# Kernel optimization log

Hardware: AMD Instinct MI355X
Metric: run time of the kernel (lower is better)

## Reference

```python
import jax, jax.numpy as jnp
import numpy as np

BN_EPS = 1e-5
CLUSTER_SIZE = 32  # K (real clusters kept after softmax)


def setup_inputs() -> dict:
    key = jax.random.key(0)
    ks = jax.random.split(key, 7)
    B, N, D, Ktot, K = 4096, 128, 512, 48, 32
    x = jax.random.normal(ks[0], (B, N, D), dtype=jnp.float32)
    clusters = jax.random.normal(ks[1], (D, Ktot), dtype=jnp.float32) / np.sqrt(D)
    bn_w = jax.random.uniform(ks[2], (Ktot,), dtype=jnp.float32)
    bn_b = jax.random.normal(ks[3], (Ktot,), dtype=jnp.float32)
    bn_rm = jax.random.normal(ks[4], (Ktot,), dtype=jnp.float32)
    bn_rv = jax.random.uniform(ks[5], (Ktot,), dtype=jnp.float32)  # positive variance
    clusters2 = jax.random.normal(ks[6], (1, D, K), dtype=jnp.float32) / np.sqrt(D)
    return {"x": x, "clusters": clusters, "bn_w": bn_w, "bn_b": bn_b,
            "bn_rm": bn_rm, "bn_rv": bn_rv, "clusters2": clusters2}


def reference(x, clusters, bn_w, bn_b, bn_rm, bn_rv, clusters2):
    # x: [B, N, D]; clusters: [D, Ktot]; clusters2: [1, D, K]
    B, N, D = x.shape
    K = clusters2.shape[-1]
    # cluster projection: [B, N, Ktot]
    logits = jnp.einsum('bnd,dk->bnk', x, clusters)
    # inference BatchNorm1d (affine with running stats)
    inv_std = jax.lax.rsqrt(bn_rv + BN_EPS)
    logits = (logits - bn_rm) * inv_std * bn_w + bn_b
    # softmax over real + ghost clusters, then drop ghost (no renorm)
    assignment = jax.nn.softmax(logits, axis=-1)[..., :K]  # [B, N, K]
    a_sum = jnp.sum(assignment, axis=1, keepdims=True)      # [B, 1, K]
    a = a_sum * clusters2                                   # [B, D, K]
    # weighted VLAD accumulate: [B, D, K]
    vlad = jnp.einsum('bnk,bnd->bdk', assignment, x) - a
    # intra-normalize (L2 across descriptor dim D, per cluster)
    vlad = vlad / jnp.maximum(jnp.linalg.norm(vlad, axis=1, keepdims=True), 1e-12)
    # flatten and L2-normalize full vector
    vlad = vlad.reshape(B, D * K)
    vlad = vlad / jnp.maximum(jnp.linalg.norm(vlad, axis=1, keepdims=True), 1e-12)
    return vlad
```

## Files before the change

### kernel.cpp

```cpp
#include <hip/hip_runtime.h>

typedef unsigned short u16;
typedef unsigned int u32;
typedef __attribute__((ext_vector_type(8))) short short8;
typedef __attribute__((ext_vector_type(4))) float f32x4;
typedef __attribute__((ext_vector_type(2))) u32 u32x2;

#define NPT 128
#define DIM 512
#define KT 48
#define KC 32

__device__ __forceinline__ u16 f2bf(float f) {
    unsigned u = __builtin_bit_cast(unsigned, f);
    return (u16)((u + 0x7FFFu + ((u >> 16) & 1u)) >> 16);
}

__device__ __forceinline__ u32 cvtpk(float lo, float hi) {
    u32 r;
    asm("v_cvt_pk_bf16_f32 %0, %1, %2" : "=v"(r) : "v"(lo), "v"(hi));
    return r;
}

__device__ __forceinline__ int swz(int n) {
    return ((n & 7) ^ ((n >> 3) & 7)) << 4;
}

__global__ void prep_kernel(const float* __restrict__ clusters,
                            const float* __restrict__ bn_w,
                            const float* __restrict__ bn_b,
                            const float* __restrict__ bn_rm,
                            const float* __restrict__ bn_rv,
                            u16* __restrict__ cTs,
                            float* __restrict__ tvec) {
    const int k = blockIdx.x;
    const float s = bn_w[k] * rsqrtf(bn_rv[k] + 1e-5f);
    if (threadIdx.x == 0) tvec[k] = bn_b[k] - bn_rm[k] * s;
    for (int d = threadIdx.x; d < DIM; d += blockDim.x)
        cTs[k * DIM + d] = f2bf(clusters[d * KT + k] * s);
}

__global__ __launch_bounds__(512)
void vlad_kernel(const float* __restrict__ x,
                 const float* __restrict__ c2,
                 const u16* __restrict__ cTs,
                 const float* __restrict__ tvec,
                 float* __restrict__ out) {
    __shared__ __align__(16) u16 xs[NPT * DIM];
    __shared__ __align__(16) u16 aT[KC][136];
    __shared__ float asum_part[8][KC];
    __shared__ float asum_s[KC];
    __shared__ float colsq_part[8][KC];
    __shared__ float scalek[KC];

    const int b    = blockIdx.x;
    const int tid  = threadIdx.x;
    const int wave = tid >> 6;
    const int lane = tid & 63;
    const int lr   = lane & 15;
    const int lg   = lane >> 4;

    {
        const float* gxw = x + (size_t)b * (NPT * DIM) + (wave * 16) * DIM;
        #pragma unroll
        for (int bt = 0; bt < 4; ++bt) {
            f32x4 tmp[8];
            #pragma unroll
            for (int i = 0; i < 8; ++i) {
                int it = bt * 8 + i;
                tmp[i] = *(const f32x4*)(gxw + (it >> 1) * DIM + (it & 1) * 256 + lane * 4);
            }
            #pragma unroll
            for (int i = 0; i < 8; ++i) {
                int it = bt * 8 + i;
                int r = wave * 16 + (it >> 1);
                u32x2 w2;
                w2[0] = cvtpk(tmp[i][0], tmp[i][1]);
                w2[1] = cvtpk(tmp[i][2], tmp[i][3]);
                int off = ((it & 1) * 512 + lane * 8) ^ swz(r);
                *(u32x2*)((char*)xs + r * 1024 + off) = w2;
            }
        }
    }

    f32x4 acc0 = {0.f,0.f,0.f,0.f}, acc1 = {0.f,0.f,0.f,0.f}, acc2 = {0.f,0.f,0.f,0.f};
    {
        const int nrow = wave * 16 + lr;
        const int rowbase = nrow * 1024;
        const int sw = swz(nrow);
        #pragma unroll 2
        for (int step = 0; step < 16; ++step) {
            const int d0 = step * 32 + lg * 8;
            short8 af = *(const short8*)((const char*)xs + (rowbase + ((2 * d0) ^ sw)));
            short8 b0 = *(const short8*)(cTs + (0 * 16 + lr) * DIM + d0);
            short8 b1 = *(const short8*)(cTs + (1 * 16 + lr) * DIM + d0);
            short8 b2 = *(const short8*)(cTs + (2 * 16 + lr) * DIM + d0);
            acc0 = __builtin_amdgcn_mfma_f32_16x16x32_bf16(af, b0, acc0, 0, 0, 0);
            acc1 = __builtin_amdgcn_mfma_f32_16x16x32_bf16(af, b1, acc1, 0, 0, 0);
            acc2 = __builtin_amdgcn_mfma_f32_16x16x32_bf16(af, b2, acc2, 0, 0, 0);
        }
    }
    {
        const float t0 = tvec[lr], t1 = tvec[16 + lr], t2 = tvec[32 + lr];
        float a0[4], a1[4];
        #pragma unroll
        for (int r = 0; r < 4; ++r) {
            float l0 = acc0[r] + t0, l1 = acc1[r] + t1, l2 = acc2[r] + t2;
            float m = fmaxf(fmaxf(l0, l1), l2);
            #pragma unroll
            for (int o = 1; o < 16; o <<= 1) m = fmaxf(m, __shfl_xor(m, o));
            float e0 = __expf(l0 - m), e1 = __expf(l1 - m), e2 = __expf(l2 - m);
            float s = e0 + e1 + e2;
            #pragma unroll
            for (int o = 1; o < 16; o <<= 1) s += __shfl_xor(s, o);
            float inv = 1.0f / s;
            a0[r] = e0 * inv; a1[r] = e1 * inv;
        }
        float p0 = 0.f, p1 = 0.f;
        #pragma unroll
        for (int r = 0; r < 4; ++r) {
            int n = wave * 16 + lg * 4 + r;
            aT[lr][n]      = f2bf(a0[r]);
            aT[16 + lr][n] = f2bf(a1[r]);
            p0 += a0[r]; p1 += a1[r];
        }
        p0 += __shfl_xor(p0, 16); p0 += __shfl_xor(p0, 32);
        p1 += __shfl_xor(p1, 16); p1 += __shfl_xor(p1, 32);
        if (lane < 16) { asum_part[wave][lane] = p0; asum_part[wave][16 + lane] = p1; }
    }
    __syncthreads();
    if (tid < KC) {
        float s = 0.f;
        #pragma unroll
        for (int w2 = 0; w2 < 8; ++w2) s += asum_part[w2][tid];
        asum_s[tid] = s;
    }

    f32x4 vacc[4][2];
    #pragma unroll
    for (int i = 0; i < 4; ++i) {
        vacc[i][0] = (f32x4){0.f,0.f,0.f,0.f};
        vacc[i][1] = (f32x4){0.f,0.f,0.f,0.f};
    }
    #pragma unroll
    for (int ns = 0; ns < 4; ++ns) {
        short8 b0 = *(const short8*)(&aT[lr][ns * 32 + lg * 8]);
        short8 b1 = *(const short8*)(&aT[16 + lr][ns * 32 + lg * 8]);
        const int n0 = ns * 32 + lg * 8;
        const int q  = (ns * 4 + lg) & 7;
        const char* pbase = (const char*)xs + n0 * 1024;
        #pragma unroll
        for (int dti = 0; dti < 4; ++dti) {
            const int d = (wave * 4 + dti) * 16 + lr;
            const int twod = 2 * d;
            short8 af;
            #pragma unroll
            for (int j = 0; j < 8; ++j)
                af[j] = *(const short*)(pbase + j * 1024 + (twod ^ ((j ^ q) << 4)));
            vacc[dti][0] = __builtin_amdgcn_mfma_f32_16x16x32_bf16(af, b0, vacc[dti][0], 0, 0, 0);
            vacc[dti][1] = __builtin_amdgcn_mfma_f32_16x16x32_bf16(af, b1, vacc[dti][1], 0, 0, 0);
        }
    }
    __syncthreads();

    float vv[4][2][4];
    float cs0 = 0.f, cs1 = 0.f;
    const float as0 = asum_s[lr], as1 = asum_s[16 + lr];
    #pragma unroll
    for (int dti = 0; dti < 4; ++dti) {
        #pragma unroll
        for (int r = 0; r < 4; ++r) {
            int d = (wave * 4 + dti) * 16 + lg * 4 + r;
            float v0 = vacc[dti][0][r] - as0 * c2[d * KC + lr];
            float v1 = vacc[dti][1][r] - as1 * c2[d * KC + 16 + lr];
            vv[dti][0][r] = v0; vv[dti][1][r] = v1;
            cs0 += v0 * v0; cs1 += v1 * v1;
        }
    }
    cs0 += __shfl_xor(cs0, 16); cs0 += __shfl_xor(cs0, 32);
    cs1 += __shfl_xor(cs1, 16); cs1 += __shfl_xor(cs1, 32);
    if (lane < 16) { colsq_part[wave][lane] = cs0; colsq_part[wave][16 + lane] = cs1; }
    __syncthreads();
    if (tid < KC) {
        float sq = 0.f;
        #pragma unroll
        for (int w2 = 0; w2 < 8; ++w2) sq += colsq_part[w2][tid];
        float cn = sqrtf(sq);
        float s1 = 1.0f / fmaxf(cn, 1e-12f);
        float c1 = cn * s1;
        float tot = c1 * c1;
        #pragma unroll
        for (int o = 1; o < 32; o <<= 1) tot += __shfl_xor(tot, o);
        scalek[tid] = s1 * (1.0f / fmaxf(sqrtf(tot), 1e-12f));
    }
    __syncthreads();
    {
        float* ob = out + (size_t)b * (DIM * KC);
        const float sk0 = scalek[lr], sk1 = scalek[16 + lr];
        #pragma unroll
        for (int dti = 0; dti < 4; ++dti) {
            #pragma unroll
            for (int r = 0; r < 4; ++r) {
                int d = (wave * 4 + dti) * 16 + lg * 4 + r;
                ob[d * KC + lr]      = vv[dti][0][r] * sk0;
                ob[d * KC + 16 + lr] = vv[dti][1][r] * sk1;
            }
        }
    }
}

extern "C" void kernel_launch(void* const* d_in, const int* in_sizes, int n_in,
                              void* d_out, int out_size, void* d_ws, size_t ws_size,
                              hipStream_t stream) {
    const float* x        = (const float*)d_in[0];
    const float* clusters = (const float*)d_in[1];
    const float* bn_w     = (const float*)d_in[2];
    const float* bn_b     = (const float*)d_in[3];
    const float* bn_rm    = (const float*)d_in[4];
    const float* bn_rv    = (const float*)d_in[5];
    const float* c2       = (const float*)d_in[6];
    float* out = (float*)d_out;

    u16*   cTs  = (u16*)d_ws;
    float* tvec = (float*)((char*)d_ws + KT * DIM * sizeof(u16));

    const int B = in_sizes[0] / (NPT * DIM);

    prep_kernel<<<KT, 256, 0, stream>>>(clusters, bn_w, bn_b, bn_rm, bn_rv, cTs, tvec);
    vlad_kernel<<<B, 512, 0, stream>>>(x, c2, cTs, tvec, out);
}
```

Baseline: 438.2 us.

## Make vlad kernel persistent over 16 batches and prefetch next batch's x

Each block now processes 16 consecutive batch elements in a loop. While the VLAD MFMA accumulation for the current element runs, the block loads the next element's x from global memory into registers, converts it to bf16 and writes it into the shared tile after a barrier. It also replaces two serial single-thread reductions with per-lane redundant reductions, removing a couple of barriers. The grid shrinks to B/16 blocks (256), each holding a 128 KB LDS tile, so the GPU may be underfilled, and the 16-entry staging registers raise register pressure.

```diff
diff --git a/kernel.cpp b/kernel.cpp
--- a/kernel.cpp
+++ b/kernel.cpp
@@ -4,12 +4,14 @@
 typedef unsigned int u32;
 typedef __attribute__((ext_vector_type(8))) short short8;
 typedef __attribute__((ext_vector_type(4))) float f32x4;
+typedef __attribute__((ext_vector_type(4))) u32 u32x4;
 typedef __attribute__((ext_vector_type(2))) u32 u32x2;
 
 #define NPT 128
 #define DIM 512
 #define KT 48
 #define KC 32
+#define BPB 16
 
 __device__ __forceinline__ u16 f2bf(float f) {
     unsigned u = __builtin_bit_cast(unsigned, f);
@@ -49,19 +51,20 @@
     __shared__ __align__(16) u16 xs[NPT * DIM];
     __shared__ __align__(16) u16 aT[KC][136];
     __shared__ float asum_part[8][KC];
-    __shared__ float asum_s[KC];
     __shared__ float colsq_part[8][KC];
-    __shared__ float scalek[KC];
-
-    const int b    = blockIdx.x;
+
     const int tid  = threadIdx.x;
     const int wave = tid >> 6;
     const int lane = tid & 63;
     const int lr   = lane & 15;
     const int lg   = lane >> 4;
 
+    const int b0i = blockIdx.x * BPB;
+
+    const float t0 = tvec[lr], t1 = tvec[16 + lr], t2 = tvec[32 + lr];
+
     {
-        const float* gxw = x + (size_t)b * (NPT * DIM) + (wave * 16) * DIM;
+        const float* gxw = x + (size_t)b0i * (NPT * DIM) + (wave * 16) * DIM;
         #pragma unroll
         for (int bt = 0; bt < 4; ++bt) {
             f32x4 tmp[8];
@@ -83,127 +86,155 @@
         }
     }
 
-    f32x4 acc0 = {0.f,0.f,0.f,0.f}, acc1 = {0.f,0.f,0.f,0.f}, acc2 = {0.f,0.f,0.f,0.f};
-    {
-        const int nrow = wave * 16 + lr;
-        const int rowbase = nrow * 1024;
-        const int sw = swz(nrow);
-        #pragma unroll 2
-        for (int step = 0; step < 16; ++step) {
-            const int d0 = step * 32 + lg * 8;
-            short8 af = *(const short8*)((const char*)xs + (rowbase + ((2 * d0) ^ sw)));
-            short8 b0 = *(const short8*)(cTs + (0 * 16 + lr) * DIM + d0);
-            short8 b1 = *(const short8*)(cTs + (1 * 16 + lr) * DIM + d0);
-            short8 b2 = *(const short8*)(cTs + (2 * 16 + lr) * DIM + d0);
-            acc0 = __builtin_amdgcn_mfma_f32_16x16x32_bf16(af, b0, acc0, 0, 0, 0);
-            acc1 = __builtin_amdgcn_mfma_f32_16x16x32_bf16(af, b1, acc1, 0, 0, 0);
-            acc2 = __builtin_amdgcn_mfma_f32_16x16x32_bf16(af, b2, acc2, 0, 0, 0);
-        }
-    }
-    {
-        const float t0 = tvec[lr], t1 = tvec[16 + lr], t2 = tvec[32 + lr];
-        float a0[4], a1[4];
-        #pragma unroll
-        for (int r = 0; r < 4; ++r) {
-            float l0 = acc0[r] + t0, l1 = acc1[r] + t1, l2 = acc2[r] + t2;
-            float m = fmaxf(fmaxf(l0, l1), l2);
-            #pragma unroll
-            for (int o = 1; o < 16; o <<= 1) m = fmaxf(m, __shfl_xor(m, o));
-            float e0 = __expf(l0 - m), e1 = __expf(l1 - m), e2 = __expf(l2 - m);
-            float s = e0 + e1 + e2;
-            #pragma unroll
-            for (int o = 1; o < 16; o <<= 1) s += __shfl_xor(s, o);
-            float inv = 1.0f / s;
-            a0[r] = e0 * inv; a1[r] = e1 * inv;
-        }
-        float p0 = 0.f, p1 = 0.f;
-        #pragma unroll
-        for (int r = 0; r < 4; ++r) {
-            int n = wave * 16 + lg * 4 + r;
-            aT[lr][n]      = f2bf(a0[r]);
-            aT[16 + lr][n] = f2bf(a1[r]);
-            p0 += a0[r]; p1 += a1[r];
-        }
-        p0 += __shfl_xor(p0, 16); p0 += __shfl_xor(p0, 32);
-        p1 += __shfl_xor(p1, 16); p1 += __shfl_xor(p1, 32);
-        if (lane < 16) { asum_part[wave][lane] = p0; asum_part[wave][16 + lane] = p1; }
-    }
-    __syncthreads();
-    if (tid < KC) {
-        float s = 0.f;
-        #pragma unroll
-        for (int w2 = 0; w2 < 8; ++w2) s += asum_part[w2][tid];
-        asum_s[tid] = s;
-    }
-
-    f32x4 vacc[4][2];
-    #pragma unroll
-    for (int i = 0; i < 4; ++i) {
-        vacc[i][0] = (f32x4){0.f,0.f,0.f,0.f};
-        vacc[i][1] = (f32x4){0.f,0.f,0.f,0.f};
-    }
-    #pragma unroll
-    for (int ns = 0; ns < 4; ++ns) {
-        short8 b0 = *(const short8*)(&aT[lr][ns * 32 + lg * 8]);
-        short8 b1 = *(const short8*)(&aT[16 + lr][ns * 32 + lg * 8]);
-        const int n0 = ns * 32 + lg * 8;
-        const int q  = (ns * 4 + lg) & 7;
-        const char* pbase = (const char*)xs + n0 * 1024;
-        #pragma unroll
-        for (int dti = 0; dti < 4; ++dti) {
-            const int d = (wave * 4 + dti) * 16 + lr;
-            const int twod = 2 * d;
-            short8 af;
-            #pragma unroll
-            for (int j = 0; j < 8; ++j)
-                af[j] = *(const short*)(pbase + j * 1024 + (twod ^ ((j ^ q) << 4)));
-            vacc[dti][0] = __builtin_amdgcn_mfma_f32_16x16x32_bf16(af, b0, vacc[dti][0], 0, 0, 0);
-            vacc[dti][1] = __builtin_amdgcn_mfma_f32_16x16x32_bf16(af, b1, vacc[dti][1], 0, 0, 0);
-        }
-    }
-    __syncthreads();
-
-    float vv[4][2][4];
-    float cs0 = 0.f, cs1 = 0.f;
-    const float as0 = asum_s[lr], as1 = asum_s[16 + lr];
-    #pragma unroll
-    for (int dti = 0; dti < 4; ++dti) {
-        #pragma unroll
-        for (int r = 0; r < 4; ++r) {
-            int d = (wave * 4 + dti) * 16 + lg * 4 + r;
-            float v0 = vacc[dti][0][r] - as0 * c2[d * KC + lr];
-            float v1 = vacc[dti][1][r] - as1 * c2[d * KC + 16 + lr];
-            vv[dti][0][r] = v0; vv[dti][1][r] = v1;
-            cs0 += v0 * v0; cs1 += v1 * v1;
-        }
-    }
-    cs0 += __shfl_xor(cs0, 16); cs0 += __shfl_xor(cs0, 32);
-    cs1 += __shfl_xor(cs1, 16); cs1 += __shfl_xor(cs1, 32);
-    if (lane < 16) { colsq_part[wave][lane] = cs0; colsq_part[wave][16 + lane] = cs1; }
-    __syncthreads();
-    if (tid < KC) {
-        float sq = 0.f;
-        #pragma unroll
-        for (int w2 = 0; w2 < 8; ++w2) sq += colsq_part[w2][tid];
-        float cn = sqrtf(sq);
-        float s1 = 1.0f / fmaxf(cn, 1e-12f);
-        float c1 = cn * s1;
-        float tot = c1 * c1;
-        #pragma unroll
-        for (int o = 1; o < 32; o <<= 1) tot += __shfl_xor(tot, o);
-        scalek[tid] = s1 * (1.0f / fmaxf(sqrtf(tot), 1e-12f));
-    }
-    __syncthreads();
-    {
-        float* ob = out + (size_t)b * (DIM * KC);
-        const float sk0 = scalek[lr], sk1 = scalek[16 + lr];
+    for (int m = 0; m < BPB; ++m) {
+        const int bm = b0i + m;
+
+        f32x4 acc0 = {0.f,0.f,0.f,0.f}, acc1 = {0.f,0.f,0.f,0.f}, acc2 = {0.f,0.f,0.f,0.f};
+        {
+            const int nrow = wave * 16 + lr;
+            const int rowbase = nrow * 1024;
+            const int sw = swz(nrow);
+            #pragma unroll 2
+            for (int step = 0; step < 16; ++step) {
+                const int d0 = step * 32 + lg * 8;
+                short8 af = *(const short8*)((const char*)xs + (rowbase + ((2 * d0) ^ sw)));
+                short8 bb0 = *(const short8*)(cTs + (0 * 16 + lr) * DIM + d0);
+                short8 bb1 = *(const short8*)(cTs + (1 * 16 + lr) * DIM + d0);
+                short8 bb2 = *(const short8*)(cTs + (2 * 16 + lr) * DIM + d0);
+                acc0 = __builtin_amdgcn_mfma_f32_16x16x32_bf16(af, bb0, acc0, 0, 0, 0);
+                acc1 = __builtin_amdgcn_mfma_f32_16x16x32_bf16(af, bb1, acc1, 0, 0, 0);
+                acc2 = __builtin_amdgcn_mfma_f32_16x16x32_bf16(af, bb2, acc2, 0, 0, 0);
+            }
+        }
+        {
+            float a0[4], a1[4];
+            #pragma unroll
+            for (int r = 0; r < 4; ++r) {
+                float l0 = acc0[r] + t0, l1 = acc1[r] + t1, l2 = acc2[r] + t2;
+                float mx = fmaxf(fmaxf(l0, l1), l2);
+                #pragma unroll
+                for (int o = 1; o < 16; o <<= 1) mx = fmaxf(mx, __shfl_xor(mx, o));
+                float e0 = __expf(l0 - mx), e1 = __expf(l1 - mx), e2 = __expf(l2 - mx);
+                float s = e0 + e1 + e2;
+                #pragma unroll
+                for (int o = 1; o < 16; o <<= 1) s += __shfl_xor(s, o);
+                float inv = 1.0f / s;
+                a0[r] = e0 * inv; a1[r] = e1 * inv;
+            }
+            float p0 = 0.f, p1 = 0.f;
+            #pragma unroll
+            for (int r = 0; r < 4; ++r) {
+                int n = wave * 16 + lg * 4 + r;
+                aT[lr][n]      = f2bf(a0[r]);
+                aT[16 + lr][n] = f2bf(a1[r]);
+                p0 += a0[r]; p1 += a1[r];
+            }
+            p0 += __shfl_xor(p0, 16); p0 += __shfl_xor(p0, 32);
+            p1 += __shfl_xor(p1, 16); p1 += __shfl_xor(p1, 32);
+            if (lane < 16) { asum_part[wave][lane] = p0; asum_part[wave][16 + lane] = p1; }
+        }
+        __syncthreads();
+
+        const int pm = (m + 1 < BPB) ? bm + 1 : bm;
+        const float* nx = x + (size_t)pm * (NPT * DIM) + (wave * 16) * DIM;
+        u32x4 stg[16];
+        f32x4 vacc[4][2];
+        #pragma unroll
+        for (int i = 0; i < 4; ++i) {
+            vacc[i][0] = (f32x4){0.f,0.f,0.f,0.f};
+            vacc[i][1] = (f32x4){0.f,0.f,0.f,0.f};
+        }
+        #pragma unroll
+        for (int ns = 0; ns < 4; ++ns) {
+            f32x4 t[8];
+            #pragma unroll
+            for (int rr = 0; rr < 4; ++rr) {
+                int i = ns * 4 + rr;
+                t[2 * rr]     = *(const f32x4*)(nx + i * DIM + lane * 8);
+                t[2 * rr + 1] = *(const f32x4*)(nx + i * DIM + lane * 8 + 4);
+            }
+            short8 bf0 = *(const short8*)(&aT[lr][ns * 32 + lg * 8]);
+            short8 bf1 = *(const short8*)(&aT[16 + lr][ns * 32 + lg * 8]);
+            const int n0 = ns * 32 + lg * 8;
+            const int q  = (ns * 4 + lg) & 7;
+            const char* pbase = (const char*)xs + n0 * 1024;
+            #pragma unroll
+            for (int dti = 0; dti < 4; ++dti) {
+                const int d = (wave * 4 + dti) * 16 + lr;
+                const int twod = 2 * d;
+                short8 af;
+                #pragma unroll
+                for (int j = 0; j < 8; ++j)
+                    af[j] = *(const short*)(pbase + j * 1024 + (twod ^ ((j ^ q) << 4)));
+                vacc[dti][0] = __builtin_amdgcn_mfma_f32_16x16x32_bf16(af, bf0, vacc[dti][0], 0, 0, 0);
+                vacc[dti][1] = __builtin_amdgcn_mfma_f32_16x16x32_bf16(af, bf1, vacc[dti][1], 0, 0, 0);
+            }
+            #pragma unroll
+            for (int rr = 0; rr < 4; ++rr) {
+                int i = ns * 4 + rr;
+                u32x4 w;
+                w[0] = cvtpk(t[2 * rr][0],     t[2 * rr][1]);
+                w[1] = cvtpk(t[2 * rr][2],     t[2 * rr][3]);
+                w[2] = cvtpk(t[2 * rr + 1][0], t[2 * rr + 1][1]);
+                w[3] = cvtpk(t[2 * rr + 1][2], t[2 * rr + 1][3]);
+                stg[i] = w;
+            }
+        }
+        __syncthreads();
+
+        #pragma unroll
+        for (int i = 0; i < 16; ++i) {
+            int r = wave * 16 + i;
+            *(u32x4*)((char*)xs + r * 1024 + ((lane * 16) ^ swz(r))) = stg[i];
+        }
+
+        float as0 = 0.f, as1 = 0.f;
+        #pragma unroll
+        for (int w2 = 0; w2 < 8; ++w2) {
+            as0 += asum_part[w2][lr];
+            as1 += asum_part[w2][16 + lr];
+        }
+        float cs0 = 0.f, cs1 = 0.f;
         #pragma unroll
         for (int dti = 0; dti < 4; ++dti) {
             #pragma unroll
             for (int r = 0; r < 4; ++r) {
                 int d = (wave * 4 + dti) * 16 + lg * 4 + r;
-                ob[d * KC + lr]      = vv[dti][0][r] * sk0;
-                ob[d * KC + 16 + lr] = vv[dti][1][r] * sk1;
+                float v0 = vacc[dti][0][r] - as0 * c2[d * KC + lr];
+                float v1 = vacc[dti][1][r] - as1 * c2[d * KC + 16 + lr];
+                vacc[dti][0][r] = v0; vacc[dti][1][r] = v1;
+                cs0 += v0 * v0; cs1 += v1 * v1;
+            }
+        }
+        cs0 += __shfl_xor(cs0, 16); cs0 += __shfl_xor(cs0, 32);
+        cs1 += __shfl_xor(cs1, 16); cs1 += __shfl_xor(cs1, 32);
+        if (lane < 16) { colsq_part[wave][lane] = cs0; colsq_part[wave][16 + lane] = cs1; }
+        __syncthreads();
+        float sq0 = 0.f, sq1 = 0.f;
+        #pragma unroll
+        for (int w2 = 0; w2 < 8; ++w2) {
+            sq0 += colsq_part[w2][lr];
+            sq1 += colsq_part[w2][16 + lr];
+        }
+        float cn0 = sqrtf(sq0), cn1 = sqrtf(sq1);
+        float s10 = 1.0f / fmaxf(cn0, 1e-12f);
+        float s11 = 1.0f / fmaxf(cn1, 1e-12f);
+        float c10 = cn0 * s10, c11 = cn1 * s11;
+        float tot = c10 * c10 + c11 * c11;
+        #pragma unroll
+        for (int o = 1; o < 16; o <<= 1) tot += __shfl_xor(tot, o);
+        float gs = 1.0f / fmaxf(sqrtf(tot), 1e-12f);
+        float sk0 = s10 * gs, sk1 = s11 * gs;
+        {
+            float* ob = out + (size_t)bm * (DIM * KC);
+            #pragma unroll
+            for (int dti = 0; dti < 4; ++dti) {
+                #pragma unroll
+                for (int r = 0; r < 4; ++r) {
+                    int d = (wave * 4 + dti) * 16 + lg * 4 + r;
+                    ob[d * KC + lr]      = vacc[dti][0][r] * sk0;
+                    ob[d * KC + 16 + lr] = vacc[dti][1][r] * sk1;
+                }
             }
         }
     }
@@ -227,5 +258,5 @@
     const int B = in_sizes[0] / (NPT * DIM);
 
     prep_kernel<<<KT, 256, 0, stream>>>(clusters, bn_w, bn_b, bn_rm, bn_rv, cTs, tvec);
-    vlad_kernel<<<B, 512, 0, stream>>>(x, c2, cTs, tvec, out);
-}
+    vlad_kernel<<<B / BPB, 512, 0, stream>>>(x, c2, cTs, tvec, out);
+}
```

After: 406.2 us. 1.08x faster.
